# Kernel tuning notes

Hardware: AMD Instinct MI355X
Metric: run time of the kernel (lower is better)

Reference implementation:

```python
import jax, jax.numpy as jnp
import numpy as np

EPS_SQUASH = 1e-6
EPS_BN = 1e-5
N_ITER = 3


def _squash(t, axis=-1):
    s = jnp.sum(t * t, axis=axis, keepdims=True)
    return s * t / ((1.0 + s) * jnp.sqrt(s + EPS_SQUASH))


def _conv(x, w, stride, pad):
    return jax.lax.conv_general_dilated(
        x, w, (stride, stride), ((pad, pad), (pad, pad)),
        dimension_numbers=('NCHW', 'OIHW', 'NCHW'))


def _bn_relu(x, g, b):
    # BatchNorm2d in training mode: batch statistics over (N,H,W), biased var
    m = jnp.mean(x, axis=(0, 2, 3), keepdims=True)
    v = jnp.var(x, axis=(0, 2, 3), keepdims=True)
    y = (x - m) / jnp.sqrt(v + EPS_BN) * g[None, :, None, None] + b[None, :, None, None]
    return jax.nn.relu(y)


def setup_inputs() -> dict:
    key = jax.random.key(0)
    ks = jax.random.split(key, 8)
    n = lambda k, shape, std: jax.random.normal(k, shape, jnp.float32) * std
    return dict(
        images=jax.random.normal(ks[0], (64, 3, 32, 32), jnp.float32),
        w1=n(ks[1], (48, 3, 3, 3), 0.1), g1=jnp.ones((48,), jnp.float32), b1=jnp.zeros((48,), jnp.float32),
        w2=n(ks[2], (96, 48, 3, 3), 0.1), g2=jnp.ones((96,), jnp.float32), b2=jnp.zeros((96,), jnp.float32),
        w3=n(ks[3], (192, 96, 3, 3), 0.1), g3=jnp.ones((192,), jnp.float32), b3=jnp.zeros((192,), jnp.float32),
        wp=n(ks[4], (192, 192, 3, 3), 0.1), bp=jnp.zeros((192,), jnp.float32),
        w_cc=n(ks[5], (144, 192, 12), 0.5),        # ConvCapsLayer weights, std=0.5 per source
        w_class=n(ks[6], (784, 10, 16, 12), 0.1),  # CapsLayer weights, std=0.1 per source
    )


def reference(images, w1, g1, b1, w2, g2, b2, w3, g3, b3, wp, bp, w_cc, w_class):
    B = images.shape[0]
    # conv stack: 32 -> 32 -> 16 -> 16
    x = _bn_relu(_conv(images, w1, 1, 1), g1, b1)
    x = _bn_relu(_conv(x, w2, 2, 1), g2, b2)
    x = _bn_relu(_conv(x, w3, 1, 1), g3, b3)
    # primary caps conv: 16 -> 7, 192 channels = 16 caps x 12 dim
    pc = _conv(x, wp, 2, 0) + bp[None, :, None, None]      # (B,192,7,7)
    u = _squash(pc.reshape(B, 784, 12))                    # (B,784,12), matches torch .view

    # ---- ConvCapsLayer (k=3, s=1, p=1) ----
    x4 = u.reshape(B, 192, 7, 7)
    xp = jnp.pad(x4, ((0, 0), (0, 0), (1, 1), (1, 1)))
    # F.unfold ordering: channel slowest, then (ki,kj), then spatial L row-major
    patches = jnp.stack([xp[:, :, i:i + 7, j:j + 7] for i in range(3) for j in range(3)], axis=2)  # (B,192,9,7,7)
    uu = patches.reshape(B, 192 * 9, 49).reshape(B, 49, 144, 12)  # faithful to torch .view reinterpretation
    u_hat = jnp.einsum('koi,btki->btko', w_cc, uu).reshape(B, 49, 144, 16, 12)
    b_log = jnp.zeros((B, 49, 144, 16, 1), jnp.float32)
    for r in range(N_ITER):
        c = jax.nn.softmax(b_log, axis=3)
        v = _squash(jnp.sum(c * u_hat, axis=2, keepdims=True))   # (B,49,1,16,12)
        if r < N_ITER - 1:
            b_log = b_log + jnp.sum(v * u_hat, axis=-1, keepdims=True)
    u2 = v.reshape(B, 784, 12)

    # ---- Class CapsLayer ----
    u_hat2 = jnp.einsum('nodi,bni->bnod', w_class, u2)           # (B,784,10,16)
    b2l = jnp.zeros((B, 784, 10, 1), jnp.float32)
    for r in range(N_ITER):
        c = jax.nn.softmax(b2l, axis=2)
        v = _squash(jnp.sum(c * u_hat2, axis=1, keepdims=True))  # (B,1,10,16)
        if r < N_ITER - 1:
            b2l = b2l + jnp.sum(v * u_hat2, axis=-1, keepdims=True)
    return v.reshape(B, 10, 16)
```

## Files before the change

### kernel.cpp

```cpp
#include <hip/hip_runtime.h>
#include <hip/hip_bf16.h>

typedef __attribute__((ext_vector_type(4))) short short4v;
typedef __attribute__((ext_vector_type(8))) short short8v;
typedef __attribute__((ext_vector_type(16))) float f32x16;

union frag8 { short8v v8; struct { short4v lo, hi; } p; };

__device__ __forceinline__ unsigned short f2bf(float v) {
  unsigned u = __float_as_uint(v);
  unsigned r = u + 0x7fffu + ((u >> 16) & 1u);
  return (unsigned short)(r >> 16);
}
__device__ __forceinline__ float bf2f(unsigned short h) {
  return __uint_as_float(((unsigned)h) << 16);
}

__global__ __launch_bounds__(192) void conv1_fused(const float* __restrict__ images,
                                                   const float* __restrict__ w1,
                                                   float* __restrict__ out) {
  int b = blockIdx.x >> 5, h = blockIdx.x & 31;
  __shared__ __align__(16) float lin[3][3][36];
  int tid = threadIdx.x;
  for (int e = tid; e < 324; e += 192) {
    int ci = e / 108, rem = e % 108, ki = rem / 36, wi = rem % 36;
    int row = h + ki - 1, col = wi - 1;
    float v = 0.f;
    if (row >= 0 && row < 32 && col >= 0 && col < 32)
      v = images[((size_t)(b*3 + ci)*32 + row)*32 + col];
    lin[ci][ki][wi] = v;
  }
  int co = tid >> 2, ws = tid & 3;
  float wr[27];
  #pragma unroll
  for (int j = 0; j < 27; ++j) wr[j] = w1[co*27 + j];
  __syncthreads();
  float o[8];
  #pragma unroll
  for (int j = 0; j < 8; ++j) o[j] = 0.f;
  #pragma unroll
  for (int ci = 0; ci < 3; ++ci)
    #pragma unroll
    for (int ki = 0; ki < 3; ++ki) {
      float4 q0 = *(const float4*)&lin[ci][ki][ws*8];
      float4 q1 = *(const float4*)&lin[ci][ki][ws*8+4];
      float4 q2 = *(const float4*)&lin[ci][ki][ws*8+8];
      float r[12] = {q0.x,q0.y,q0.z,q0.w,q1.x,q1.y,q1.z,q1.w,q2.x,q2.y,q2.z,q2.w};
      #pragma unroll
      for (int kj = 0; kj < 3; ++kj) {
        float wv = wr[(ci*3+ki)*3+kj];
        #pragma unroll
        for (int j = 0; j < 8; ++j) o[j] = fmaf(r[j+kj], wv, o[j]);
      }
    }
  float* dst = out + (((size_t)(b*48+co)*32 + h)*32 + ws*8);
  *(float4*)dst       = make_float4(o[0],o[1],o[2],o[3]);
  *(float4*)(dst + 4) = make_float4(o[4],o[5],o[6],o[7]);
}

__device__ __forceinline__ void split_one(const float* w, unsigned short* wh,
                                          unsigned short* wl, int CI, int i) {
  int K = CI*9;
  int co = i / K, rem = i % K, tap = rem / CI, ci = rem % CI;
  float v = w[(co*CI + ci)*9 + tap];
  unsigned short h = f2bf(v);
  wh[i] = h;
  wl[i] = f2bf(v - bf2f(h));
}
__global__ void split_w_all(const float* __restrict__ w2, const float* __restrict__ w3,
                            const float* __restrict__ wp,
                            unsigned short* wh2, unsigned short* wl2,
                            unsigned short* wh3, unsigned short* wl3,
                            unsigned short* whp, unsigned short* wlp) {
  int i = blockIdx.x*256 + threadIdx.x;
  if (i < 41472) split_one(w2, wh2, wl2, 48, i);
  else if (i < 207360) split_one(w3, wh3, wl3, 96, i - 41472);
  else if (i < 539136) split_one(wp, whp, wlp, 192, i - 207360);
}

template<int C,int H,int W,int P>
__global__ void bn_split_nhwc(const float* __restrict__ in, const float* __restrict__ sc,
                              unsigned short* __restrict__ xh, unsigned short* __restrict__ xl) {
  constexpr int HP = H + 2*P, WP = W + 2*P;
  int b = blockIdx.x / HP, hp = blockIdx.x % HP;
  int h = hp - P;
  for (int e = threadIdx.x; e < WP*C; e += 256) {
    int wp = e / C, c = e % C;
    int w = wp - P;
    float v = 0.f;
    if (h >= 0 && h < H && w >= 0 && w < W) {
      v = in[((size_t)(b*C + c)*H + h)*W + w];
      v = fmaf(v, sc[c*2], sc[c*2+1]);
      v = v > 0.f ? v : 0.f;
    }
    unsigned short hh = f2bf(v);
    size_t o = ((size_t)(b*HP + hp)*WP + wp)*C + c;
    xh[o] = hh;
    xl[o] = f2bf(v - bf2f(hh));
  }
}

template<int CI,int HIP,int WIP,int HO,int WO,int STR,int SPLITK>
__global__ __launch_bounds__(256,4) void conv_mfma(
    const unsigned short* __restrict__ xh, const unsigned short* __restrict__ xl,
    const unsigned short* __restrict__ wh, const unsigned short* __restrict__ wl,
    float* __restrict__ part, int CO, int B) {
  constexpr int K = CI*9, NSP = HO*WO, KCH = K/SPLITK, LDA = 36;
  const int NTOT = B*NSP;
  const int m0 = blockIdx.x*64, n0 = blockIdx.y*128, ks = blockIdx.z;
  __shared__ unsigned short Ah[64*LDA], Al[64*LDA], Bh[128*LDA], Bl[128*LDA];
  const int tid = threadIdx.x, lane = tid & 63, wid = tid >> 6;
  const int wm = wid >> 1, wn = wid & 1;
  const int arow = tid >> 2, ak0 = (tid & 3)*8;
  const bool aok = (m0 + arow) < CO;
  const size_t abase = (size_t)(m0 + arow)*K;
  int brow[2], bk0[2];
  size_t bbase[2];
  #pragma unroll
  for (int i = 0; i < 2; ++i) {
    int e = tid + i*256;
    brow[i] = e >> 2; bk0[i] = (e & 3)*8;
    int nn = n0 + brow[i]; if (nn > NTOT-1) nn = NTOT-1;
    int bb = nn / NSP, sp = nn % NSP;
    int ho = sp / WO, wo = sp % WO;
    bbase[i] = ((size_t)bb*HIP + ho*STR)*WIP + wo*STR;
  }
  f32x16 acc0 = (f32x16)0.f, acc1 = (f32x16)0.f;
  const int kBeg = ks*KCH, kEnd = kBeg + KCH;
  for (int kc = kBeg; kc < kEnd; kc += 32) {
    const int kLim = (kEnd - kc) < 32 ? (kEnd - kc) : 32;
    {
      frag8 vh, vl;
      vh.v8 = (short8v)(short)0; vl.v8 = (short8v)(short)0;
      if (aok && ak0 < kLim) {
        size_t off = abase + kc + ak0;
        vh.v8 = *(const short8v*)(wh + off);
        vl.v8 = *(const short8v*)(wl + off);
      }
      int lo_ = arow*LDA + ak0;
      *(short4v*)(Ah + lo_) = vh.p.lo; *(short4v*)(Ah + lo_ + 4) = vh.p.hi;
      *(short4v*)(Al + lo_) = vl.p.lo; *(short4v*)(Al + lo_ + 4) = vl.p.hi;
    }
    #pragma unroll
    for (int i = 0; i < 2; ++i) {
      frag8 vh, vl;
      vh.v8 = (short8v)(short)0; vl.v8 = (short8v)(short)0;
      if (bk0[i] < kLim) {
        int kg = kc + bk0[i];
        int tap = kg / CI, ci0 = kg - tap*CI;
        int dh = tap / 3, dw = tap - dh*3;
        size_t off = (bbase[i] + (size_t)dh*WIP + dw)*CI + ci0;
        vh.v8 = *(const short8v*)(xh + off);
        vl.v8 = *(const short8v*)(xl + off);
      }
      int lo_ = brow[i]*LDA + bk0[i];
      *(short4v*)(Bh + lo_) = vh.p.lo; *(short4v*)(Bh + lo_ + 4) = vh.p.hi;
      *(short4v*)(Bl + lo_) = vl.p.lo; *(short4v*)(Bl + lo_ + 4) = vl.p.hi;
    }
    __syncthreads();
    #pragma unroll
    for (int kst = 0; kst < 2; ++kst) {
      const int kb = kst*16 + 8*(lane >> 5);
      const int ar = wm*32 + (lane & 31);
      frag8 ah, al;
      { int o = ar*LDA + kb;
        ah.p.lo = *(const short4v*)(Ah + o); ah.p.hi = *(const short4v*)(Ah + o + 4);
        al.p.lo = *(const short4v*)(Al + o); al.p.hi = *(const short4v*)(Al + o + 4); }
      const int br = wn*64 + (lane & 31);
      frag8 bh0, bl0, bh1, bl1;
      { int o = br*LDA + kb;
        bh0.p.lo = *(const short4v*)(Bh + o); bh0.p.hi = *(const short4v*)(Bh + o + 4);
        bl0.p.lo = *(const short4v*)(Bl + o); bl0.p.hi = *(const short4v*)(Bl + o + 4); }
      { int o = (br+32)*LDA + kb;
        bh1.p.lo = *(const short4v*)(Bh + o); bh1.p.hi = *(const short4v*)(Bh + o + 4);
        bl1.p.lo = *(const short4v*)(Bl + o); bl1.p.hi = *(const short4v*)(Bl + o + 4); }
      acc0 = __builtin_amdgcn_mfma_f32_32x32x16_bf16(ah.v8, bh0.v8, acc0, 0, 0, 0);
      acc0 = __builtin_amdgcn_mfma_f32_32x32x16_bf16(ah.v8, bl0.v8, acc0, 0, 0, 0);
      acc0 = __builtin_amdgcn_mfma_f32_32x32x16_bf16(al.v8, bh0.v8, acc0, 0, 0, 0);
      acc1 = __builtin_amdgcn_mfma_f32_32x32x16_bf16(ah.v8, bh1.v8, acc1, 0, 0, 0);
      acc1 = __builtin_amdgcn_mfma_f32_32x32x16_bf16(ah.v8, bl1.v8, acc1, 0, 0, 0);
      acc1 = __builtin_amdgcn_mfma_f32_32x32x16_bf16(al.v8, bh1.v8, acc1, 0, 0, 0);
    }
    __syncthreads();
  }
  #pragma unroll
  for (int ns = 0; ns < 2; ++ns) {
    f32x16 a = ns ? acc1 : acc0;
    #pragma unroll
    for (int r = 0; r < 16; ++r) {
      int row = (r & 3) + 8*(r >> 2) + 4*(lane >> 5);
      int m = m0 + wm*32 + row;
      int n = n0 + wn*64 + ns*32 + (lane & 31);
      if (m < CO && n < NTOT) {
        if (SPLITK == 1) {
          int b = n / NSP, sp = n % NSP;
          part[((size_t)b*CO + m)*NSP + sp] = a[r];
        } else {
          part[((size_t)ks*CO + m)*NTOT + n] = a[r];
        }
      }
    }
  }
}

template<int CO,int NSP,int SPLITK,bool BIAS,bool STATS>
__global__ void splitk_reduce(const float* __restrict__ part, const float* __restrict__ bias,
                              float* __restrict__ out, float* __restrict__ stats, int B) {
  const int NTOT = B*NSP;
  int i = blockIdx.x*256 + threadIdx.x;
  bool valid = i < CO*NTOT;
  float s = 0.f;
  if (valid) {
    int co = i / NTOT, n = i % NTOT;
    #pragma unroll
    for (int ks = 0; ks < SPLITK; ++ks) s += part[(size_t)(ks*CO + co)*NTOT + n];
    if (BIAS) s += bias[co];
    int b = n / NSP, sp = n % NSP;
    out[((size_t)b*CO + co)*NSP + sp] = s;
  }
  if (STATS) {
    float sum = valid ? s : 0.f, sq = valid ? s*s : 0.f;
    #pragma unroll
    for (int off = 32; off; off >>= 1) {
      sum += __shfl_down(sum, off, 64);
      sq  += __shfl_down(sq,  off, 64);
    }
    __shared__ float ls[2][4];
    int lane = threadIdx.x & 63, wv = threadIdx.x >> 6;
    if (lane == 0) { ls[0][wv] = sum; ls[1][wv] = sq; }
    __syncthreads();
    if (threadIdx.x == 0) {
      float S = 0.f, Q = 0.f;
      #pragma unroll
      for (int j = 0; j < 4; ++j) { S += ls[0][j]; Q += ls[1][j]; }
      int bpc = NTOT/256;
      int co = blockIdx.x / bpc, slice = blockIdx.x % bpc;
      stats[(co*bpc + slice)*2 + 0] = S;
      stats[(co*bpc + slice)*2 + 1] = Q;
    }
  }
}

template<int C,int HW,int SLICES>
__global__ void bn_partial(const float* __restrict__ x, float* __restrict__ part, int B) {
  int c = blockIdx.x / SLICES, s = blockIdx.x % SLICES;
  int bpp = B / SLICES;
  float sum = 0.f, sq = 0.f;
  for (int b = s*bpp; b < (s+1)*bpp; ++b) {
    const float* p = x + ((size_t)b*C + c)*HW;
    for (int i = threadIdx.x; i < HW; i += blockDim.x) {
      float v = p[i]; sum += v; sq += v*v;
    }
  }
  #pragma unroll
  for (int off = 32; off; off >>= 1) {
    sum += __shfl_down(sum, off, 64);
    sq  += __shfl_down(sq,  off, 64);
  }
  __shared__ float ls[2][4];
  int lane = threadIdx.x & 63, wv = threadIdx.x >> 6;
  if (lane == 0) { ls[0][wv] = sum; ls[1][wv] = sq; }
  __syncthreads();
  if (threadIdx.x == 0) {
    float S = 0.f, Q = 0.f;
    #pragma unroll
    for (int i = 0; i < 4; ++i) { S += ls[0][i]; Q += ls[1][i]; }
    part[(c*SLICES+s)*2+0] = S; part[(c*SLICES+s)*2+1] = Q;
  }
}

template<int C,int SLICES>
__global__ void bn_final(const float* __restrict__ part, const float* __restrict__ g,
                         const float* __restrict__ bta, float* __restrict__ sc, int NHW) {
  int c = blockIdx.x*blockDim.x + threadIdx.x;
  if (c >= C) return;
  float S = 0.f, Q = 0.f;
  for (int s = 0; s < SLICES; ++s) { S += part[(c*SLICES+s)*2]; Q += part[(c*SLICES+s)*2+1]; }
  float m = S / NHW, v = Q / NHW - m*m;
  float inv = rsqrtf(v + 1e-5f);
  float a = g[c] * inv;
  sc[c*2] = a; sc[c*2+1] = bta[c] - m*a;
}

__global__ void squash_pc(float* __restrict__ pc, int ncaps) {
  int i = blockIdx.x*blockDim.x + threadIdx.x;
  if (i >= ncaps) return;
  float* p = pc + (size_t)i*12;
  float v[12]; float s = 0.f;
  #pragma unroll
  for (int d = 0; d < 12; ++d) { v[d] = p[d]; s += v[d]*v[d]; }
  float sc = s / ((1.f + s)*sqrtf(s + 1e-6f));
  #pragma unroll
  for (int d = 0; d < 12; ++d) p[d] = v[d]*sc;
}

__global__ void uu_gather(const float* __restrict__ sq, float* __restrict__ uu, int B) {
  int idx = blockIdx.x*blockDim.x + threadIdx.x;
  int total = B*49*144*12;
  if (idx >= total) return;
  int ii = idx % 12; int t0 = idx / 12;
  int kk = t0 % 144; t0 /= 144;
  int tt = t0 % 49;  int b = t0 / 49;
  int f = tt*1728 + kk*12 + ii;
  int c = f / 441; int r = f - c*441;
  int k = r / 49;  int sp = r - k*49;
  int y = sp / 7, x = sp - y*7;
  int iy = y + k/3 - 1, ix = x + (k%3) - 1;
  float val = 0.f;
  if (iy >= 0 && iy < 7 && ix >= 0 && ix < 7)
    val = sq[((size_t)(b*192 + c)*7 + iy)*7 + ix];
  uu[idx] = val;
}

__global__ __launch_bounds__(192) void cc_einsum2(const float* __restrict__ uu,
                                                  const float* __restrict__ wcc,
                                                  __hip_bfloat16* __restrict__ uhat,
                                                  int row0, int nrows) {
  int k  = blockIdx.x;
  int m0 = blockIdx.y * 64;
  int o = threadIdx.x;
  const float4* wp4 = (const float4*)(wcc + ((size_t)k*192 + o)*12);
  float4 w0 = wp4[0], w1 = wp4[1], w2 = wp4[2];
  int mmax = nrows - m0; if (mmax > 64) mmax = 64;
  #pragma unroll 2
  for (int m = 0; m < mmax; ++m) {
    const float4* ar = (const float4*)(uu + ((size_t)(row0+m0+m)*144 + k)*12);
    float4 a0 = ar[0], a1 = ar[1], a2 = ar[2];
    float acc = a0.x*w0.x + a0.y*w0.y + a0.z*w0.z + a0.w*w0.w
              + a1.x*w1.x + a1.y*w1.y + a1.z*w1.z + a1.w*w1.w
              + a2.x*w2.x + a2.y*w2.y + a2.z*w2.z + a2.w*w2.w;
    uhat[((size_t)(m0+m)*144 + k)*192 + o] = __float2bfloat16(acc);
  }
}

__global__ __launch_bounds__(256) void cc_route(const __hip_bfloat16* __restrict__ uhat,
                                                float* __restrict__ u2, int rowOff) {
  const int row = blockIdx.x;
  const unsigned short* __restrict__ uh = (const unsigned short*)uhat + (size_t)row*27648;
  __shared__ float red[16][192];
  __shared__ float sraw[192];
  __shared__ float vsh[192];
  const int tid = threadIdx.x;
  const int g = tid >> 4, oc = tid & 15;
  const unsigned short* __restrict__ ubase = uh + oc*12;
  float blog[9];
  #pragma unroll
  for (int j = 0; j < 9; ++j) blog[j] = 0.f;
  float sacc[12];

  for (int r = 0; r < 3; ++r) {
    #pragma unroll
    for (int d = 0; d < 12; ++d) sacc[d] = 0.f;
    float vq[12];
    if (r > 0) {
      #pragma unroll
      for (int d = 0; d < 12; ++d) vq[d] = vsh[oc*12 + d];
    }
    for (int j = 0; j < 9; ++j) {
      const unsigned short* up = ubase + (g + 16*j)*192;
      uint2 q0 = *(const uint2*)up;
      uint2 q1 = *(const uint2*)(up + 4);
      uint2 q2 = *(const uint2*)(up + 8);
      float uf[12];
      uf[0] = bf2f((unsigned short)(q0.x & 0xffff)); uf[1] = bf2f((unsigned short)(q0.x >> 16));
      uf[2] = bf2f((unsigned short)(q0.y & 0xffff)); uf[3] = bf2f((unsigned short)(q0.y >> 16));
      uf[4] = bf2f((unsigned short)(q1.x & 0xffff)); uf[5] = bf2f((unsigned short)(q1.x >> 16));
      uf[6] = bf2f((unsigned short)(q1.y & 0xffff)); uf[7] = bf2f((unsigned short)(q1.y >> 16));
      uf[8] = bf2f((unsigned short)(q2.x & 0xffff)); uf[9] = bf2f((unsigned short)(q2.x >> 16));
      uf[10] = bf2f((unsigned short)(q2.y & 0xffff)); uf[11] = bf2f((unsigned short)(q2.y >> 16));
      if (r == 0) {
        #pragma unroll
        for (int d = 0; d < 12; ++d) sacc[d] += uf[d];
      } else {
        float dot = 0.f;
        #pragma unroll
        for (int d = 0; d < 12; ++d) dot = fmaf(vq[d], uf[d], dot);
        blog[j] += dot;
        float mx = blog[j];
        #pragma unroll
        for (int off = 1; off < 16; off <<= 1) mx = fmaxf(mx, __shfl_xor(mx, off, 16));
        float e = __expf(blog[j] - mx);
        float es = e;
        #pragma unroll
        for (int off = 1; off < 16; off <<= 1) es += __shfl_xor(es, off, 16);
        float c = e / es;
        #pragma unroll
        for (int d = 0; d < 12; ++d) sacc[d] = fmaf(c, uf[d], sacc[d]);
      }
    }
    #pragma unroll
    for (int d = 0; d < 12; ++d) red[g][oc*12 + d] = sacc[d];
    __syncthreads();
    if (tid < 192) {
      float s = 0.f;
      #pragma unroll
      for (int q = 0; q < 16; ++q) s += red[q][tid];
      if (r == 0) s *= 0.0625f;
      sraw[tid] = s;
    }
    __syncthreads();
    if (tid < 192) {
      int qc = tid / 12;
      float nrm = 0.f;
      #pragma unroll
      for (int d = 0; d < 12; ++d) { float v = sraw[qc*12 + d]; nrm += v*v; }
      float sc = nrm / ((1.f + nrm)*sqrtf(nrm + 1e-6f));
      vsh[tid] = sraw[tid]*sc;
    }
    __syncthreads();
  }
  if (tid < 192) u2[((size_t)(rowOff + row))*192 + tid] = vsh[tid];
}

__global__ void class_einsum(const float* __restrict__ u2, const float* __restrict__ wcl,
                             unsigned short* __restrict__ uhat2, int B) {
  int n = blockIdx.x;
  __shared__ float u2l[64][12];
  int tid = threadIdx.x;
  for (int e = tid; e < 64*12; e += 320) {
    int b = e / 12, i = e % 12;
    u2l[b][i] = u2[(size_t)b*9408 + n*12 + i];
  }
  __syncthreads();
  int od = tid % 160, bh = tid / 160;
  int o = od >> 4, d = od & 15;
  float w[12];
  #pragma unroll
  for (int i = 0; i < 12; ++i) w[i] = wcl[(size_t)n*1920 + o*192 + d*12 + i];
  for (int b = bh*32; b < bh*32+32; ++b) {
    float acc = 0.f;
    #pragma unroll
    for (int i = 0; i < 12; ++i) acc = fmaf(w[i], u2l[b][i], acc);
    uhat2[((size_t)b*784 + n)*160 + od] = f2bf(acc);
  }
}

template<int MODE>
__global__ __launch_bounds__(256) void cls_pass(const unsigned short* __restrict__ uh2b,
                                                const float* __restrict__ vprev,
                                                float* __restrict__ b2l,
                                                float* __restrict__ cpart) {
  const int b = blockIdx.x, sl = blockIdx.y;
  const int tid = threadIdx.x, lane = tid & 63, wv = tid >> 6;
  const int nl = lane >> 4, d = lane & 15;
  float v[10];
  if (MODE != 0) {
    #pragma unroll
    for (int o = 0; o < 10; ++o) v[o] = vprev[b*160 + o*16 + d];
  }
  float sacc[10];
  #pragma unroll
  for (int o = 0; o < 10; ++o) sacc[o] = 0.f;
  for (int step = 0; step < 7; ++step) {
    const int n = sl*112 + step*16 + wv*4 + nl;
    const unsigned short* up = uh2b + ((size_t)b*784 + n)*160 + d;
    float u[10];
    #pragma unroll
    for (int o = 0; o < 10; ++o) u[o] = bf2f(up[o*16]);
    if (MODE == 0) {
      #pragma unroll
      for (int o = 0; o < 10; ++o) sacc[o] += u[o];
    } else {
      float bb[10];
      #pragma unroll
      for (int o = 0; o < 10; ++o) {
        float t = v[o]*u[o];
        #pragma unroll
        for (int off = 8; off; off >>= 1) t += __shfl_xor(t, off, 16);
        bb[o] = t;
      }
      if (MODE == 2) {
        #pragma unroll
        for (int o = 0; o < 10; ++o) bb[o] += b2l[((size_t)b*784 + n)*10 + o];
      }
      if (MODE == 1 && d < 10) b2l[((size_t)b*784 + n)*10 + d] = bb[d];
      float mx = bb[0];
      #pragma unroll
      for (int o = 1; o < 10; ++o) mx = fmaxf(mx, bb[o]);
      float es = 0.f;
      #pragma unroll
      for (int o = 0; o < 10; ++o) { bb[o] = __expf(bb[o]-mx); es += bb[o]; }
      float inv = 1.f/es;
      #pragma unroll
      for (int o = 0; o < 10; ++o) sacc[o] = fmaf(bb[o]*inv, u[o], sacc[o]);
    }
  }
  #pragma unroll
  for (int o = 0; o < 10; ++o) {
    sacc[o] += __shfl_xor(sacc[o], 16, 64);
    sacc[o] += __shfl_xor(sacc[o], 32, 64);
  }
  __shared__ float red[4][160];
  if (lane < 16) {
    #pragma unroll
    for (int o = 0; o < 10; ++o) red[wv][o*16 + d] = sacc[o];
  }
  __syncthreads();
  if (tid < 160) {
    float s = red[0][tid] + red[1][tid] + red[2][tid] + red[3][tid];
    cpart[((size_t)b*7 + sl)*160 + tid] = s;
  }
}

__global__ __launch_bounds__(160) void cls_finish(const float* __restrict__ cpart,
                                                  float* __restrict__ vout, float fac) {
  int b = blockIdx.x, od = threadIdx.x;
  float s = 0.f;
  #pragma unroll
  for (int sl = 0; sl < 7; ++sl) s += cpart[((size_t)b*7 + sl)*160 + od];
  s *= fac;
  float nrm = s*s;
  #pragma unroll
  for (int off = 8; off; off >>= 1) nrm += __shfl_xor(nrm, off, 16);
  float sc = nrm / ((1.f + nrm)*sqrtf(nrm + 1e-6f));
  vout[(size_t)b*160 + od] = s*sc;
}

extern "C" void kernel_launch(void* const* d_in, const int* in_sizes, int n_in,
                              void* d_out, int out_size, void* d_ws, size_t ws_size,
                              hipStream_t stream) {
  const float* images = (const float*)d_in[0];
  const float* w1  = (const float*)d_in[1];
  const float* g1  = (const float*)d_in[2];
  const float* b1  = (const float*)d_in[3];
  const float* w2  = (const float*)d_in[4];
  const float* g2  = (const float*)d_in[5];
  const float* b2  = (const float*)d_in[6];
  const float* w3  = (const float*)d_in[7];
  const float* g3  = (const float*)d_in[8];
  const float* b3  = (const float*)d_in[9];
  const float* wp  = (const float*)d_in[10];
  const float* bp  = (const float*)d_in[11];
  const float* wcc = (const float*)d_in[12];
  const float* wcl = (const float*)d_in[13];
  float* out = (float*)d_out;
  float* ws  = (float*)d_ws;

  float* t1    = ws + 0;
  float* t2    = ws + 3145728;
  float* t3    = ws + 4718592;
  float* pc    = ws + 7864320;
  float* uu    = ws + 8466432;
  float* u2b   = ws + 13885440;
  unsigned short* uh2b = (unsigned short*)(ws + 14487552);
  float* b2l   = ws + 22515712;
  float* scrC  = ws + 23017472;
  float* v2    = ws + 23519232;
  float* spart = ws + 23529472;
  float* ssc1  = ws + 23532544;
  float* ssc2  = ws + 23532640;
  float* ssc3  = ws + 23532832;
  float* U     = ws + 23533312;
  __hip_bfloat16* uhc = (__hip_bfloat16*)(ws + 34371328);

  unsigned short* wh2 = (unsigned short*)(uu + 0);
  unsigned short* wl2 = (unsigned short*)(uu + 20736);
  unsigned short* wh3 = (unsigned short*)(uu + 41472);
  unsigned short* wl3 = (unsigned short*)(uu + 124416);
  unsigned short* whp = (unsigned short*)(uu + 207360);
  unsigned short* wlp = (unsigned short*)(uu + 373248);

  unsigned short* x2h = (unsigned short*)(U + 0);
  unsigned short* x2l = (unsigned short*)(U + 1775616);
  float*          part2 = U + 3551232;
  unsigned short* x3h = (unsigned short*)(U + 0);
  unsigned short* x3l = (unsigned short*)(U + 995328);
  unsigned short* xph = (unsigned short*)(U + 0);
  unsigned short* xpl = (unsigned short*)(U + 1572864);
  float*          partp = U + 3145728;

  const int B = 64;

  split_w_all<<<2106,256,0,stream>>>(w2, w3, wp, wh2, wl2, wh3, wl3, whp, wlp);

  conv1_fused<<<2048,192,0,stream>>>(images, w1, t1);
  bn_partial<48,1024,8><<<48*8,256,0,stream>>>(t1, spart, B);
  bn_final<48,8><<<1,64,0,stream>>>(spart, g1, b1, ssc1, 65536);

  bn_split_nhwc<48,32,32,1><<<64*34,256,0,stream>>>(t1, ssc1, x2h, x2l);
  conv_mfma<48,34,34,16,16,2,3><<<dim3(2,128,3),256,0,stream>>>(x2h, x2l, wh2, wl2, part2, 96, B);
  splitk_reduce<96,256,3,false,true><<<6144,256,0,stream>>>(part2, nullptr, t2, scrC, B);
  bn_final<96,64><<<1,128,0,stream>>>(scrC, g2, b2, ssc2, 16384);

  bn_split_nhwc<96,16,16,1><<<64*18,256,0,stream>>>(t2, ssc2, x3h, x3l);
  conv_mfma<96,18,18,16,16,1,1><<<dim3(3,128,1),256,0,stream>>>(x3h, x3l, wh3, wl3, t3, 192, B);
  bn_partial<192,256,8><<<192*8,256,0,stream>>>(t3, spart, B);
  bn_final<192,8><<<1,192,0,stream>>>(spart, g3, b3, ssc3, 16384);

  bn_split_nhwc<192,16,16,0><<<64*16,256,0,stream>>>(t3, ssc3, xph, xpl);
  conv_mfma<192,16,16,7,7,2,8><<<dim3(3,25,8),256,0,stream>>>(xph, xpl, whp, wlp, partp, 192, B);
  splitk_reduce<192,49,8,true,false><<<2352,256,0,stream>>>(partp, bp, pc, nullptr, B);
  squash_pc<<<196,256,0,stream>>>(pc, 50176);

  uu_gather<<<21168,256,0,stream>>>(pc, uu, B);
  for (int cb = 0; cb < 2; ++cb) {
    cc_einsum2<<<dim3(144,25),192,0,stream>>>(uu, wcc, uhc, cb*1568, 1568);
    cc_route<<<1568,256,0,stream>>>(uhc, u2b, cb*1568);
  }
  class_einsum<<<784,320,0,stream>>>(u2b, wcl, uh2b, B);
  cls_pass<0><<<dim3(64,7),256,0,stream>>>(uh2b, v2, b2l, scrC);
  cls_finish<<<64,160,0,stream>>>(scrC, v2, 0.1f);
  cls_pass<1><<<dim3(64,7),256,0,stream>>>(uh2b, v2, b2l, scrC);
  cls_finish<<<64,160,0,stream>>>(scrC, v2, 1.0f);
  cls_pass<2><<<dim3(64,7),256,0,stream>>>(uh2b, v2, b2l, scrC);
  cls_finish<<<64,160,0,stream>>>(scrC, out, 1.0f);
  (void)in_sizes; (void)n_in; (void)out_size; (void)ws_size;
}
```

Before: 399.0 us.

## Cache routing u_hat row in LDS and reduce partial sums via wave shuffles

The cc_route kernel now copies each row's bf16 u_hat tile into shared memory during the first routing iteration and rereads it from LDS in later iterations instead of global memory. The cross-group partial-sum reduction first combines partials within each wave using xor shuffles, which shrinks the shared reduction buffer from 16 to 4 rows. The j loop is fully unrolled and launch bounds request 2 blocks per CU. The cost is about 56 KB of LDS per block, which limits occupancy, and if the tile was already served from cache, the gain from avoiding global rereads may be small.

```diff
diff --git a/kernel.cpp b/kernel.cpp
--- a/kernel.cpp
+++ b/kernel.cpp
@@ -333,34 +333,42 @@
   }
 }
 
-__global__ __launch_bounds__(256) void cc_route(const __hip_bfloat16* __restrict__ uhat,
-                                                float* __restrict__ u2, int rowOff) {
+__global__ __launch_bounds__(256,2) void cc_route(const __hip_bfloat16* __restrict__ uhat,
+                                                  float* __restrict__ u2, int rowOff) {
   const int row = blockIdx.x;
   const unsigned short* __restrict__ uh = (const unsigned short*)uhat + (size_t)row*27648;
-  __shared__ float red[16][192];
+  __shared__ __align__(16) unsigned short uhl[144*196];
+  __shared__ float red[4][192];
   __shared__ float sraw[192];
   __shared__ float vsh[192];
-  const int tid = threadIdx.x;
+  const int tid = threadIdx.x, lane = tid & 63, wv = tid >> 6;
   const int g = tid >> 4, oc = tid & 15;
-  const unsigned short* __restrict__ ubase = uh + oc*12;
   float blog[9];
   #pragma unroll
   for (int j = 0; j < 9; ++j) blog[j] = 0.f;
-  float sacc[12];
 
   for (int r = 0; r < 3; ++r) {
-    #pragma unroll
-    for (int d = 0; d < 12; ++d) sacc[d] = 0.f;
     float vq[12];
     if (r > 0) {
       #pragma unroll
       for (int d = 0; d < 12; ++d) vq[d] = vsh[oc*12 + d];
     }
+    float sacc[12];
+    #pragma unroll
+    for (int d = 0; d < 12; ++d) sacc[d] = 0.f;
+    #pragma unroll
     for (int j = 0; j < 9; ++j) {
-      const unsigned short* up = ubase + (g + 16*j)*192;
-      uint2 q0 = *(const uint2*)up;
-      uint2 q1 = *(const uint2*)(up + 4);
-      uint2 q2 = *(const uint2*)(up + 8);
+      const int k = g + 16*j;
+      uint2 q0, q1, q2;
+      if (r == 0) {
+        const unsigned short* up = uh + k*192 + oc*12;
+        q0 = *(const uint2*)up; q1 = *(const uint2*)(up + 4); q2 = *(const uint2*)(up + 8);
+        unsigned short* lp = uhl + k*196 + oc*12;
+        *(uint2*)lp = q0; *(uint2*)(lp + 4) = q1; *(uint2*)(lp + 8) = q2;
+      } else {
+        const unsigned short* lp = uhl + k*196 + oc*12;
+        q0 = *(const uint2*)lp; q1 = *(const uint2*)(lp + 4); q2 = *(const uint2*)(lp + 8);
+      }
       float uf[12];
       uf[0] = bf2f((unsigned short)(q0.x & 0xffff)); uf[1] = bf2f((unsigned short)(q0.x >> 16));
       uf[2] = bf2f((unsigned short)(q0.y & 0xffff)); uf[3] = bf2f((unsigned short)(q0.y >> 16));
@@ -389,12 +397,17 @@
       }
     }
     #pragma unroll
-    for (int d = 0; d < 12; ++d) red[g][oc*12 + d] = sacc[d];
+    for (int d = 0; d < 12; ++d) {
+      sacc[d] += __shfl_xor(sacc[d], 16, 64);
+      sacc[d] += __shfl_xor(sacc[d], 32, 64);
+    }
+    if (lane < 16) {
+      #pragma unroll
+      for (int d = 0; d < 12; ++d) red[wv][oc*12 + d] = sacc[d];
+    }
     __syncthreads();
     if (tid < 192) {
-      float s = 0.f;
-      #pragma unroll
-      for (int q = 0; q < 16; ++q) s += red[q][tid];
+      float s = red[0][tid] + red[1][tid] + red[2][tid] + red[3][tid];
       if (r == 0) s *= 0.0625f;
       sraw[tid] = s;
     }
```

After: 384.6 us. 3.6% less time.
